# Kernel optimization log

Measured on AMD Instinct MI355X. Metric: run time of the kernel, lower is better.

The kernel has to match this reference:

```python
import jax, jax.numpy as jnp
import numpy as np

D = 512
H = 8
G = 4          # GroupNorm groups
EPS = 1e-3     # GroupNorm eps


def group_norm(x):
    # x: (b, n, t, d); torch code normalizes per (batch, group) over (n*t, d/G)
    b, n, t, d = x.shape
    xr = x.reshape(b, n * t, G, d // G)
    mu = xr.mean(axis=(1, 3), keepdims=True)
    var = ((xr - mu) ** 2).mean(axis=(1, 3), keepdims=True)
    return ((xr - mu) * jax.lax.rsqrt(var + EPS)).reshape(b, n, t, d)


def setup_inputs() -> dict:
    key = jax.random.key(0)
    ks = jax.random.split(key, 9)
    s = 1.0 / np.sqrt(D)
    inp = {
        "ind": 0,
        "in_f": jax.random.normal(ks[0], (4, 8, 512, D), dtype=jnp.float32),
        "in_f_kv": jax.random.normal(ks[1], (4, 8, 512, D), dtype=jnp.float32),
        "Wq": jax.random.normal(ks[2], (D, D), dtype=jnp.float32) * s,
        "Wk": jax.random.normal(ks[3], (D, D), dtype=jnp.float32) * s,
        "Wv": jax.random.normal(ks[4], (D, D), dtype=jnp.float32) * s,
        "Wz": jax.random.normal(ks[5], (D, D), dtype=jnp.float32) * s,
        "bz": jnp.zeros((D,), dtype=jnp.float32),
        "W1": jax.random.normal(ks[6], (D, D), dtype=jnp.float32) * s,
        "b1": jnp.full((D,), 0.1, dtype=jnp.float32),
        "W2": jax.random.normal(ks[7], (D, D), dtype=jnp.float32) * s,
        "b2": jnp.full((D,), 0.1, dtype=jnp.float32),
    }
    return inp


def reference(ind, in_f, in_f_kv, Wq, Wk, Wv, Wz, bz, W1, b1, W2, b2):
    b, n, t, d = in_f.shape
    hd = d // H
    scale = 1.0 / np.sqrt(hd)

    _in_f = group_norm(in_f)          # LN_1
    _in_f_kv = group_norm(in_f_kv)    # LN_2

    # torch Linear: y = x @ W.T
    q = group_norm(_in_f @ Wq.T)      # LN_3
    k = group_norm(_in_f_kv @ Wk.T)   # LN_4
    v = _in_f_kv @ Wv.T

    q = q.reshape(b, n, t, H, hd)
    k = k.reshape(b, n, -1, H, hd)
    v = v.reshape(b, n, -1, H, hd)

    logits = jnp.einsum('bnqhd,bnkhd->bnhqk', q, k) * scale
    attn_weights = jax.nn.softmax(logits, axis=-1)
    attn_out = jnp.einsum('bnhqk,bnkhd->bnqhd', attn_weights, v).reshape(b, n, t, d)

    in_f_u1 = attn_out @ Wz.T + bz
    in_f_u2 = jax.nn.leaky_relu(_in_f @ W1.T + b1, negative_slope=0.01) @ W2.T + b2

    out_f = in_f + in_f_u1 + in_f_u2
    return (out_f, attn_weights)
```

## Files before the change

kernel.cpp:

```cpp
#include <hip/hip_runtime.h>
#include <math.h>

#define TDIM 512
#define DDIM 512
#define NTROWS 4096
#define MROWS 16384
#define EPSGN 1e-3f

typedef __attribute__((ext_vector_type(8))) short bf16x8;
typedef __attribute__((ext_vector_type(4))) float f32x4;
typedef __attribute__((ext_vector_type(8))) unsigned short us8;
typedef __attribute__((ext_vector_type(4))) unsigned short us4;

__device__ __forceinline__ unsigned short f2b(float f) {
  unsigned int u = __float_as_uint(f);
  return (unsigned short)((u + 0x7fffu + ((u >> 16) & 1u)) >> 16);
}
__device__ __forceinline__ float b2f(unsigned short h) {
  return __uint_as_float(((unsigned int)h) << 16);
}

#define GLOAD16(g, l)                                                                   \
  __builtin_amdgcn_global_load_lds((const __attribute__((address_space(1))) void*)(g),  \
                                   (__attribute__((address_space(3))) void*)(l), 16, 0, 0)

__global__ __launch_bounds__(256) void gn_stats_partial(const float* __restrict__ x,
                                                        float* __restrict__ part) {
  const int grp = blockIdx.x;
  const int chunk = blockIdx.y;
  const int b = grp >> 2, g = grp & 3;
  const float* base = x + (size_t)b * NTROWS * DDIM + g * 128;
  const int r0 = chunk * (NTROWS / 32);
  float s = 0.f, sq = 0.f;
  for (int i = threadIdx.x; i < 128 * 32; i += 256) {
    const int r = i >> 5, c4 = (i & 31) << 2;
    const float4 v = *(const float4*)(base + (size_t)(r0 + r) * DDIM + c4);
    s += v.x + v.y + v.z + v.w;
    sq += v.x * v.x + v.y * v.y + v.z * v.z + v.w * v.w;
  }
#pragma unroll
  for (int o = 32; o > 0; o >>= 1) { s += __shfl_down(s, o); sq += __shfl_down(sq, o); }
  __shared__ float red[8];
  const int wid = threadIdx.x >> 6;
  if ((threadIdx.x & 63) == 0) { red[wid * 2] = s; red[wid * 2 + 1] = sq; }
  __syncthreads();
  if (threadIdx.x == 0) {
    float S = 0.f, SQ = 0.f;
    for (int w = 0; w < 4; ++w) { S += red[w * 2]; SQ += red[w * 2 + 1]; }
    part[(grp * 32 + chunk) * 2] = S;
    part[(grp * 32 + chunk) * 2 + 1] = SQ;
  }
}

__global__ __launch_bounds__(256) void cvt_gn(const float* __restrict__ x,
                                              const float* __restrict__ part,
                                              unsigned short* __restrict__ o) {
  __shared__ float sstat[32];
  if (threadIdx.x < 16) {
    const float* p = part + threadIdx.x * 64;
    float S = 0.f, SQ = 0.f;
    for (int c = 0; c < 32; ++c) { S += p[c * 2]; SQ += p[c * 2 + 1]; }
    const float inv = 1.f / (float)(NTROWS * 128);
    const float mu = S * inv;
    const float var = SQ * inv - mu * mu;
    sstat[threadIdx.x * 2] = mu;
    sstat[threadIdx.x * 2 + 1] = rsqrtf(var + EPSGN);
  }
  __syncthreads();
  const int NC = MROWS * DDIM / 8;
  for (int c = blockIdx.x * 256 + threadIdx.x; c < NC; c += gridDim.x * 256) {
    const int e = c * 8;
    const int row = e >> 9;
    const int ch = e & 511;
    const int sidx = (((row >> 12) << 2) | (ch >> 7)) << 1;
    const float mu = sstat[sidx], rs = sstat[sidx + 1];
    const float4 f0 = *(const float4*)(x + (size_t)e);
    const float4 f1 = *(const float4*)(x + (size_t)e + 4);
    us8 v;
    v[0] = f2b((f0.x - mu) * rs); v[1] = f2b((f0.y - mu) * rs);
    v[2] = f2b((f0.z - mu) * rs); v[3] = f2b((f0.w - mu) * rs);
    v[4] = f2b((f1.x - mu) * rs); v[5] = f2b((f1.y - mu) * rs);
    v[6] = f2b((f1.z - mu) * rs); v[7] = f2b((f1.w - mu) * rs);
    *(us8*)(o + (size_t)e) = v;
  }
}

__global__ __launch_bounds__(256) void cvt_w(const float* w0, const float* w1, const float* w2,
                                             const float* w3, const float* w4, const float* w5,
                                             unsigned short* __restrict__ dst) {
  const float* s;
  switch (blockIdx.y) {
    case 0: s = w0; break; case 1: s = w1; break; case 2: s = w2; break;
    case 3: s = w3; break; case 4: s = w4; break; default: s = w5; break;
  }
  unsigned short* d = dst + (size_t)blockIdx.y * 262144;
  const int c = blockIdx.x * 256 + threadIdx.x;
  const float4 f0 = *(const float4*)(s + (size_t)c * 8);
  const float4 f1 = *(const float4*)(s + (size_t)c * 8 + 4);
  us8 o;
  o[0] = f2b(f0.x); o[1] = f2b(f0.y); o[2] = f2b(f0.z); o[3] = f2b(f0.w);
  o[4] = f2b(f1.x); o[5] = f2b(f1.y); o[6] = f2b(f1.z); o[7] = f2b(f1.w);
  *(us8*)(d + (size_t)c * 8) = o;
}

template <int EPI, int STATS>
__global__ __launch_bounds__(256) void gemm_bf16(const unsigned short* __restrict__ A,
                                                 const unsigned short* __restrict__ B,
                                                 unsigned short* __restrict__ Cb,
                                                 const float* __restrict__ bias,
                                                 float* __restrict__ part) {
  __shared__ __align__(16) unsigned short As[128 * 64];
  __shared__ __align__(16) unsigned short Bs[128 * 64];
  const int tid = threadIdx.x;
  const int wave = tid >> 6, lane = tid & 63;
  const int bm = blockIdx.x << 7, bn = blockIdx.y << 7;
  const int wr = (wave >> 1) << 6;
  const int wc = (wave & 1) << 6;
  const int lr = lane & 15, lg = lane >> 4;

  f32x4 acc[4][4] = {};

  const int srow = lane >> 3;
  const int sslot = (lane & 7) ^ srow;

  for (int k0 = 0; k0 < 512; k0 += 64) {
    __syncthreads();
#pragma unroll
    for (int i = 0; i < 4; ++i) {
      const int ci = wave * 4 + i;
      const int row = ci * 8 + srow;
      GLOAD16(A + (size_t)(bm + row) * 512 + k0 + sslot * 8, (char*)As + ci * 1024);
      GLOAD16(B + (size_t)(bn + row) * 512 + k0 + sslot * 8, (char*)Bs + ci * 1024);
    }
    __syncthreads();
#pragma unroll
    for (int kk = 0; kk < 64; kk += 32) {
      bf16x8 af[4], bfr[4];
#pragma unroll
      for (int i = 0; i < 4; ++i) {
        const int row = wr + i * 16 + lr;
        af[i] = *(const bf16x8*)&As[row * 64 + ((((kk >> 3) + lg) ^ (row & 7)) << 3)];
      }
#pragma unroll
      for (int j = 0; j < 4; ++j) {
        const int row = wc + j * 16 + lr;
        bfr[j] = *(const bf16x8*)&Bs[row * 64 + ((((kk >> 3) + lg) ^ (row & 7)) << 3)];
      }
#pragma unroll
      for (int i = 0; i < 4; ++i)
#pragma unroll
        for (int j = 0; j < 4; ++j)
          acc[i][j] = __builtin_amdgcn_mfma_f32_16x16x32_bf16(af[i], bfr[j], acc[i][j], 0, 0, 0);
    }
  }

#pragma unroll
  for (int i = 0; i < 4; ++i) {
    const int row0 = bm + wr + i * 16 + lg * 4;
#pragma unroll
    for (int j = 0; j < 4; ++j) {
      const int col = bn + wc + j * 16 + lr;
      if (EPI == 0) {
#pragma unroll
        for (int r = 0; r < 4; ++r)
          Cb[(size_t)(row0 + r) * 512 + col] = f2b(acc[i][j][r]);
      } else if (EPI == 1) {
        const float bb = bias[col];
#pragma unroll
        for (int r = 0; r < 4; ++r) {
          float v = acc[i][j][r] + bb;
          v = v > 0.f ? v : 0.01f * v;
          Cb[(size_t)(row0 + r) * 512 + col] = f2b(v);
        }
      } else {
        us4 pk;
#pragma unroll
        for (int r = 0; r < 4; ++r) pk[r] = f2b(acc[i][j][r]);
        *(us4*)&Cb[((size_t)(row0 >> 9) * 512 + col) * 512 + (row0 & 511)] = pk;
      }
    }
  }

  if (STATS) {
    float s = 0.f, sq = 0.f;
#pragma unroll
    for (int i = 0; i < 4; ++i)
#pragma unroll
      for (int j = 0; j < 4; ++j)
#pragma unroll
        for (int r = 0; r < 4; ++r) { const float v = acc[i][j][r]; s += v; sq += v * v; }
#pragma unroll
    for (int o = 32; o > 0; o >>= 1) { s += __shfl_xor(s, o); sq += __shfl_xor(sq, o); }
    __shared__ float red[8];
    if (lane == 0) { red[wave * 2] = s; red[wave * 2 + 1] = sq; }
    __syncthreads();
    if (tid == 0) {
      const float S = red[0] + red[2] + red[4] + red[6];
      const float SQ = red[1] + red[3] + red[5] + red[7];
      const int batch = blockIdx.x >> 5, slot = blockIdx.x & 31, g = blockIdx.y;
      const int idx = ((((batch << 2) | g) << 5) | slot) << 1;
      part[idx] = S;
      part[idx + 1] = SQ;
    }
  }
}

__global__ __launch_bounds__(256) void gemm_final(const unsigned short* __restrict__ A0,
                                                  const unsigned short* __restrict__ A1,
                                                  const unsigned short* __restrict__ B0,
                                                  const unsigned short* __restrict__ B1,
                                                  float* __restrict__ Cf,
                                                  const float* __restrict__ bias0,
                                                  const float* __restrict__ bias1,
                                                  const float* __restrict__ init) {
  __shared__ __align__(16) unsigned short As[128 * 64];
  __shared__ __align__(16) unsigned short Bs[128 * 64];
  const int tid = threadIdx.x;
  const int wave = tid >> 6, lane = tid & 63;
  const int bm = blockIdx.x << 7, bn = blockIdx.y << 7;
  const int wr = (wave >> 1) << 6;
  const int wc = (wave & 1) << 6;
  const int lr = lane & 15, lg = lane >> 4;

  f32x4 acc[4][4] = {};
  const int srow = lane >> 3;
  const int sslot = (lane & 7) ^ srow;

  for (int k0 = 0; k0 < 1024; k0 += 64) {
    const unsigned short* Ab = (k0 < 512) ? A0 : A1;
    const unsigned short* Bb = (k0 < 512) ? B0 : B1;
    const int kl = k0 & 511;
    __syncthreads();
#pragma unroll
    for (int i = 0; i < 4; ++i) {
      const int ci = wave * 4 + i;
      const int row = ci * 8 + srow;
      GLOAD16(Ab + (size_t)(bm + row) * 512 + kl + sslot * 8, (char*)As + ci * 1024);
      GLOAD16(Bb + (size_t)(bn + row) * 512 + kl + sslot * 8, (char*)Bs + ci * 1024);
    }
    __syncthreads();
#pragma unroll
    for (int kk = 0; kk < 64; kk += 32) {
      bf16x8 af[4], bfr[4];
#pragma unroll
      for (int i = 0; i < 4; ++i) {
        const int row = wr + i * 16 + lr;
        af[i] = *(const bf16x8*)&As[row * 64 + ((((kk >> 3) + lg) ^ (row & 7)) << 3)];
      }
#pragma unroll
      for (int j = 0; j < 4; ++j) {
        const int row = wc + j * 16 + lr;
        bfr[j] = *(const bf16x8*)&Bs[row * 64 + ((((kk >> 3) + lg) ^ (row & 7)) << 3)];
      }
#pragma unroll
      for (int i = 0; i < 4; ++i)
#pragma unroll
        for (int j = 0; j < 4; ++j)
          acc[i][j] = __builtin_amdgcn_mfma_f32_16x16x32_bf16(af[i], bfr[j], acc[i][j], 0, 0, 0);
    }
  }

#pragma unroll
  for (int i = 0; i < 4; ++i) {
    const int row0 = bm + wr + i * 16 + lg * 4;
#pragma unroll
    for (int j = 0; j < 4; ++j) {
      const int col = bn + wc + j * 16 + lr;
      const float bb = bias0[col] + bias1[col];
#pragma unroll
      for (int r = 0; r < 4; ++r) {
        const size_t o = (size_t)(row0 + r) * 512 + col;
        Cf[o] = acc[i][j][r] + bb + init[o];
      }
    }
  }
}

__global__ __launch_bounds__(256) void attn_fused(const unsigned short* __restrict__ q16,
                                                  const unsigned short* __restrict__ k16,
                                                  const unsigned short* __restrict__ vT,
                                                  const float* __restrict__ part_q,
                                                  const float* __restrict__ part_k,
                                                  float* __restrict__ aw,
                                                  unsigned short* __restrict__ ao16) {
  __shared__ __align__(16) unsigned short Qs[64 * 64];
  __shared__ __align__(16) unsigned short Ks[256 * 64];
  __shared__ __align__(16) unsigned short Ps[64 * 256];
  __shared__ float WM[4][64];
  __shared__ float WS[4][64];
  __shared__ float sstat[4];

  const int bid = blockIdx.x;
  const int q0 = blockIdx.y << 6;
  const int h = bid & 7;
  const int b = bid >> 6;
  const int tid = threadIdx.x;
  const int w = tid >> 6, lane = tid & 63;
  const int lr = lane & 15, lg = lane >> 4;

  if (tid < 2) {
    const float* p = (tid == 0 ? part_q : part_k) + ((((b << 2) | (h >> 1)) << 5) << 1);
    float S = 0.f, SQ = 0.f;
    for (int c = 0; c < 32; ++c) { S += p[c * 2]; SQ += p[c * 2 + 1]; }
    const float inv = 1.f / (float)(NTROWS * 128);
    const float mu = S * inv;
    const float var = SQ * inv - mu * mu;
    sstat[tid * 2] = mu;
    sstat[tid * 2 + 1] = rsqrtf(var + EPSGN);
  }
  __syncthreads();
  const float qmu = sstat[0], qrs = sstat[1], kmu = sstat[2], krs = sstat[3];

  const size_t hb = (size_t)(bid >> 3) * (512 * 512);
  const unsigned short* Qg = q16 + hb + h * 64;
  const unsigned short* Kg = k16 + hb + h * 64;
  const unsigned short* Vg = vT + hb + (size_t)h * 64 * 512;

  {
    const int row = tid >> 2, cb = (tid & 3) << 4;
    const us8 v0 = *(const us8*)(Qg + (size_t)(q0 + row) * 512 + cb);
    const us8 v1 = *(const us8*)(Qg + (size_t)(q0 + row) * 512 + cb + 8);
    us8 o0, o1;
#pragma unroll
    for (int j = 0; j < 8; ++j) {
      o0[j] = f2b((b2f(v0[j]) - qmu) * qrs);
      o1[j] = f2b((b2f(v1[j]) - qmu) * qrs);
    }
    const int s0 = (cb >> 3) ^ (row & 7);
    const int s1 = ((cb >> 3) + 1) ^ (row & 7);
    *(us8*)&Qs[row * 64 + (s0 << 3)] = o0;
    *(us8*)&Qs[row * 64 + (s1 << 3)] = o1;
  }

  f32x4 sc[4][8] = {};

#pragma unroll
  for (int half = 0; half < 2; ++half) {
    __syncthreads();
#pragma unroll
    for (int it = 0; it < 8; ++it) {
      const int row = it * 32 + (tid >> 3), slot = tid & 7;
      const us8 v = *(const us8*)(Kg + (size_t)(half * 256 + row) * 512 + (slot << 3));
      us8 o;
#pragma unroll
      for (int j = 0; j < 8; ++j) o[j] = f2b((b2f(v[j]) - kmu) * krs);
      *(us8*)&Ks[row * 64 + ((slot ^ (row & 7)) << 3)] = o;
    }
    __syncthreads();
#pragma unroll
    for (int kk = 0; kk < 64; kk += 32) {
      bf16x8 aq[4];
#pragma unroll
      for (int qf = 0; qf < 4; ++qf) {
        const int row = qf * 16 + lr;
        aq[qf] = *(const bf16x8*)&Qs[row * 64 + ((((kk >> 3) + lg) ^ (row & 7)) << 3)];
      }
#pragma unroll
      for (int kf = 0; kf < 4; ++kf) {
        const int row = w * 64 + kf * 16 + lr;
        const bf16x8 bk = *(const bf16x8*)&Ks[row * 64 + ((((kk >> 3) + lg) ^ (row & 7)) << 3)];
#pragma unroll
        for (int qf = 0; qf < 4; ++qf)
          sc[qf][half * 4 + kf] =
              __builtin_amdgcn_mfma_f32_16x16x32_bf16(aq[qf], bk, sc[qf][half * 4 + kf], 0, 0, 0);
      }
    }
  }

  float Mv[4][4];
#pragma unroll
  for (int qf = 0; qf < 4; ++qf)
#pragma unroll
    for (int r = 0; r < 4; ++r) {
      float m = sc[qf][0][r];
#pragma unroll
      for (int kf = 1; kf < 8; ++kf) m = fmaxf(m, sc[qf][kf][r]);
#pragma unroll
      for (int o = 1; o < 16; o <<= 1) m = fmaxf(m, __shfl_xor(m, o));
      Mv[qf][r] = m;
    }
  if (lr == 0) {
#pragma unroll
    for (int qf = 0; qf < 4; ++qf)
#pragma unroll
      for (int r = 0; r < 4; ++r) WM[w][qf * 16 + lg * 4 + r] = Mv[qf][r];
  }
  __syncthreads();
#pragma unroll
  for (int qf = 0; qf < 4; ++qf)
#pragma unroll
    for (int r = 0; r < 4; ++r) {
      const int q = qf * 16 + lg * 4 + r;
      Mv[qf][r] = fmaxf(fmaxf(WM[0][q], WM[1][q]), fmaxf(WM[2][q], WM[3][q]));
    }
  float sl[4][4] = {};
#pragma unroll
  for (int qf = 0; qf < 4; ++qf)
#pragma unroll
    for (int kf = 0; kf < 8; ++kf) {
      f32x4 v = sc[qf][kf];
#pragma unroll
      for (int r = 0; r < 4; ++r) {
        const float e = __expf((v[r] - Mv[qf][r]) * 0.125f);
        v[r] = e;
        sl[qf][r] += e;
      }
      sc[qf][kf] = v;
    }
#pragma unroll
  for (int qf = 0; qf < 4; ++qf)
#pragma unroll
    for (int r = 0; r < 4; ++r) {
      float s = sl[qf][r];
#pragma unroll
      for (int o = 1; o < 16; o <<= 1) s += __shfl_xor(s, o);
      sl[qf][r] = s;
    }
  if (lr == 0) {
#pragma unroll
    for (int qf = 0; qf < 4; ++qf)
#pragma unroll
      for (int r = 0; r < 4; ++r) WS[w][qf * 16 + lg * 4 + r] = sl[qf][r];
  }
  __syncthreads();
#pragma unroll
  for (int qf = 0; qf < 4; ++qf)
#pragma unroll
    for (int r = 0; r < 4; ++r) {
      const int q = qf * 16 + lg * 4 + r;
      const float inv = 1.f / (WS[0][q] + WS[1][q] + WS[2][q] + WS[3][q]);
#pragma unroll
      for (int kf = 0; kf < 8; ++kf) sc[qf][kf][r] *= inv;
    }

  float* AWp = aw + ((size_t)bid * 512 + q0) * 512;
#pragma unroll
  for (int qf = 0; qf < 4; ++qf)
#pragma unroll
    for (int kfi = 0; kfi < 8; ++kfi) {
      const int k = ((kfi >> 2) << 8) + w * 64 + ((kfi & 3) << 4) + lr;
#pragma unroll
      for (int r = 0; r < 4; ++r)
        AWp[(size_t)(qf * 16 + lg * 4 + r) * 512 + k] = sc[qf][kfi][r];
    }

  f32x4 accO[4] = {};
#pragma unroll
  for (int half = 0; half < 2; ++half) {
    __syncthreads();
#pragma unroll
    for (int it = 0; it < 8; ++it) {
      const int ci = w * 8 + it;
      const int row = ci * 2 + (lane >> 5);
      const int s = lane & 31;
      GLOAD16(Vg + (size_t)row * 512 + half * 256 + ((s ^ (row & 7)) << 3),
              (char*)Ks + ci * 1024);
    }
#pragma unroll
    for (int qf = 0; qf < 4; ++qf)
#pragma unroll
      for (int r = 0; r < 4; ++r) {
        const int q = qf * 16 + lg * 4 + r;
#pragma unroll
        for (int kf = 0; kf < 4; ++kf) {
          const int k = w * 64 + (kf << 4) + lr;
          Ps[q * 256 + (((k >> 3) ^ (q & 7)) << 3) + (k & 7)] = f2b(sc[qf][half * 4 + kf][r]);
        }
      }
    __syncthreads();
#pragma unroll
    for (int ks = 0; ks < 256; ks += 32) {
      const int sl0 = ks >> 3;
      const int q = w * 16 + lr;
      const bf16x8 af = *(const bf16x8*)&Ps[q * 256 + (((sl0 + lg) ^ (q & 7)) << 3)];
#pragma unroll
      for (int df = 0; df < 4; ++df) {
        const int row = df * 16 + lr;
        const bf16x8 vb = *(const bf16x8*)&Ks[row * 256 + (((sl0 + lg) ^ (row & 7)) << 3)];
        accO[df] = __builtin_amdgcn_mfma_f32_16x16x32_bf16(af, vb, accO[df], 0, 0, 0);
      }
    }
  }

  const int growb = (bid >> 3) * 512 + q0 + w * 16 + lg * 4;
#pragma unroll
  for (int df = 0; df < 4; ++df)
#pragma unroll
    for (int r = 0; r < 4; ++r)
      ao16[(size_t)(growb + r) * 512 + h * 64 + df * 16 + lr] = f2b(accO[df][r]);
}

extern "C" void kernel_launch(void* const* d_in, const int* in_sizes, int n_in,
                              void* d_out, int out_size, void* d_ws, size_t ws_size,
                              hipStream_t stream) {
  const float* in_f = (const float*)d_in[1];
  const float* in_fkv = (const float*)d_in[2];
  const float* Wq = (const float*)d_in[3];
  const float* Wk = (const float*)d_in[4];
  const float* Wv = (const float*)d_in[5];
  const float* Wz = (const float*)d_in[6];
  const float* bz = (const float*)d_in[7];
  const float* W1 = (const float*)d_in[8];
  const float* b1 = (const float*)d_in[9];
  const float* W2 = (const float*)d_in[10];
  const float* b2 = (const float*)d_in[11];

  float* out_f = (float*)d_out;
  float* attw = out_f + (size_t)MROWS * DDIM;

  const size_t TSB = (size_t)MROWS * DDIM;
  unsigned short* us = (unsigned short*)d_ws;
  unsigned short* a16 = us;
  unsigned short* akv16 = us + TSB;
  unsigned short* q16 = us + 2 * TSB;
  unsigned short* k16 = us + 3 * TSB;
  unsigned short* h16 = us + 4 * TSB;
  unsigned short* ao16 = us + 5 * TSB;
  unsigned short* vT = us + 6 * TSB;
  unsigned short* w16 = us + 7 * TSB;
  float* fbase = (float*)(us + 7 * TSB + 6 * 262144);
  float* part0 = fbase;
  float* part1 = fbase + 1024;
  float* part_q = fbase + 2048;
  float* part_k = fbase + 3072;

  dim3 sg(16, 32);
  gn_stats_partial<<<sg, 256, 0, stream>>>(in_f, part0);
  gn_stats_partial<<<sg, 256, 0, stream>>>(in_fkv, part1);
  cvt_gn<<<2048, 256, 0, stream>>>(in_f, part0, a16);
  cvt_gn<<<2048, 256, 0, stream>>>(in_fkv, part1, akv16);
  cvt_w<<<dim3(128, 6), 256, 0, stream>>>(Wq, Wk, Wv, Wz, W1, W2, w16);

  dim3 gg(128, 4);
  gemm_bf16<0, 1><<<gg, 256, 0, stream>>>(a16, w16 + 0 * 262144, q16, nullptr, part_q);
  gemm_bf16<0, 1><<<gg, 256, 0, stream>>>(akv16, w16 + 1 * 262144, k16, nullptr, part_k);
  gemm_bf16<2, 0><<<gg, 256, 0, stream>>>(akv16, w16 + 2 * 262144, vT, nullptr, nullptr);
  gemm_bf16<1, 0><<<gg, 256, 0, stream>>>(a16, w16 + 4 * 262144, h16, b1, nullptr);

  attn_fused<<<dim3(256, 8), 256, 0, stream>>>(q16, k16, vT, part_q, part_k, attw, ao16);

  gemm_final<<<gg, 256, 0, stream>>>(ao16, h16, w16 + 3 * 262144, w16 + 5 * 262144, out_f, bz,
                                     b2, in_f);
}
```

Baseline: 287.1 us.

## Batch paired launches and move Q/K GroupNorm out of attention into separate pass

Merges the two stats and two convert launches into single launches that pick their inputs by grid index, and fuses the four projection GEMMs into two paired launches that share an A operand across a doubled grid. Q/K group normalization moves out of the attention kernel into a standalone in-place norm_qk pass. The attention kernel can then load Q and K tiles straight into LDS with async global-to-LDS loads. This cuts launch overhead and per-block normalization work inside attention, at the cost of an extra read-write pass over q16 and k16.

```diff
diff --git a/kernel.cpp b/kernel.cpp
--- a/kernel.cpp
+++ b/kernel.cpp
@@ -24,8 +24,12 @@
   __builtin_amdgcn_global_load_lds((const __attribute__((address_space(1))) void*)(g),  \
                                    (__attribute__((address_space(3))) void*)(l), 16, 0, 0)
 
-__global__ __launch_bounds__(256) void gn_stats_partial(const float* __restrict__ x,
-                                                        float* __restrict__ part) {
+__global__ __launch_bounds__(256) void gn_stats_partial(const float* __restrict__ x0,
+                                                        const float* __restrict__ x1,
+                                                        float* __restrict__ p0,
+                                                        float* __restrict__ p1) {
+  const float* x = blockIdx.z ? x1 : x0;
+  float* part = blockIdx.z ? p1 : p0;
   const int grp = blockIdx.x;
   const int chunk = blockIdx.y;
   const int b = grp >> 2, g = grp & 3;
@@ -52,9 +56,15 @@
   }
 }
 
-__global__ __launch_bounds__(256) void cvt_gn(const float* __restrict__ x,
-                                              const float* __restrict__ part,
-                                              unsigned short* __restrict__ o) {
+__global__ __launch_bounds__(256) void cvt_gn(const float* __restrict__ x0,
+                                              const float* __restrict__ x1,
+                                              const float* __restrict__ p0,
+                                              const float* __restrict__ p1,
+                                              unsigned short* __restrict__ o0,
+                                              unsigned short* __restrict__ o1) {
+  const float* x = blockIdx.y ? x1 : x0;
+  const float* part = blockIdx.y ? p1 : p0;
+  unsigned short* o = blockIdx.y ? o1 : o0;
   __shared__ float sstat[32];
   if (threadIdx.x < 16) {
     const float* p = part + threadIdx.x * 64;
@@ -103,23 +113,27 @@
   *(us8*)(d + (size_t)c * 8) = o;
 }
 
-template <int EPI, int STATS>
-__global__ __launch_bounds__(256) void gemm_bf16(const unsigned short* __restrict__ A,
-                                                 const unsigned short* __restrict__ B,
-                                                 unsigned short* __restrict__ Cb,
+template <int PAIR>
+__global__ __launch_bounds__(256) void gemm_pair(const unsigned short* __restrict__ A,
+                                                 const unsigned short* __restrict__ B0,
+                                                 const unsigned short* __restrict__ B1,
+                                                 unsigned short* __restrict__ C0,
+                                                 unsigned short* __restrict__ C1,
                                                  const float* __restrict__ bias,
                                                  float* __restrict__ part) {
   __shared__ __align__(16) unsigned short As[128 * 64];
   __shared__ __align__(16) unsigned short Bs[128 * 64];
   const int tid = threadIdx.x;
   const int wave = tid >> 6, lane = tid & 63;
-  const int bm = blockIdx.x << 7, bn = blockIdx.y << 7;
+  const int bm = blockIdx.x << 7;
+  const bool first = blockIdx.y < 4;
+  const unsigned short* B = first ? B0 : B1;
+  const int bnl = (blockIdx.y & 3) << 7;
   const int wr = (wave >> 1) << 6;
   const int wc = (wave & 1) << 6;
   const int lr = lane & 15, lg = lane >> 4;
 
   f32x4 acc[4][4] = {};
-
   const int srow = lane >> 3;
   const int sslot = (lane & 7) ^ srow;
 
@@ -130,7 +144,7 @@
       const int ci = wave * 4 + i;
       const int row = ci * 8 + srow;
       GLOAD16(A + (size_t)(bm + row) * 512 + k0 + sslot * 8, (char*)As + ci * 1024);
-      GLOAD16(B + (size_t)(bn + row) * 512 + k0 + sslot * 8, (char*)Bs + ci * 1024);
+      GLOAD16(B + (size_t)(bnl + row) * 512 + k0 + sslot * 8, (char*)Bs + ci * 1024);
     }
     __syncthreads();
 #pragma unroll
@@ -154,34 +168,18 @@
     }
   }
 
-#pragma unroll
-  for (int i = 0; i < 4; ++i) {
-    const int row0 = bm + wr + i * 16 + lg * 4;
-#pragma unroll
-    for (int j = 0; j < 4; ++j) {
-      const int col = bn + wc + j * 16 + lr;
-      if (EPI == 0) {
+  if (first) {
+#pragma unroll
+    for (int i = 0; i < 4; ++i) {
+      const int row0 = bm + wr + i * 16 + lg * 4;
+#pragma unroll
+      for (int j = 0; j < 4; ++j) {
+        const int col = bnl + wc + j * 16 + lr;
 #pragma unroll
         for (int r = 0; r < 4; ++r)
-          Cb[(size_t)(row0 + r) * 512 + col] = f2b(acc[i][j][r]);
-      } else if (EPI == 1) {
-        const float bb = bias[col];
-#pragma unroll
-        for (int r = 0; r < 4; ++r) {
-          float v = acc[i][j][r] + bb;
-          v = v > 0.f ? v : 0.01f * v;
-          Cb[(size_t)(row0 + r) * 512 + col] = f2b(v);
-        }
-      } else {
-        us4 pk;
-#pragma unroll
-        for (int r = 0; r < 4; ++r) pk[r] = f2b(acc[i][j][r]);
-        *(us4*)&Cb[((size_t)(row0 >> 9) * 512 + col) * 512 + (row0 & 511)] = pk;
-      }
-    }
-  }
-
-  if (STATS) {
+          C0[(size_t)(row0 + r) * 512 + col] = f2b(acc[i][j][r]);
+      }
+    }
     float s = 0.f, sq = 0.f;
 #pragma unroll
     for (int i = 0; i < 4; ++i)
@@ -202,7 +200,65 @@
       part[idx] = S;
       part[idx + 1] = SQ;
     }
-  }
+  } else if (PAIR == 0) {
+#pragma unroll
+    for (int i = 0; i < 4; ++i) {
+      const int row0 = bm + wr + i * 16 + lg * 4;
+#pragma unroll
+      for (int j = 0; j < 4; ++j) {
+        const int col = bnl + wc + j * 16 + lr;
+        const float bb = bias[col];
+#pragma unroll
+        for (int r = 0; r < 4; ++r) {
+          float v = acc[i][j][r] + bb;
+          v = v > 0.f ? v : 0.01f * v;
+          C1[(size_t)(row0 + r) * 512 + col] = f2b(v);
+        }
+      }
+    }
+  } else {
+#pragma unroll
+    for (int i = 0; i < 4; ++i) {
+      const int row0 = bm + wr + i * 16 + lg * 4;
+#pragma unroll
+      for (int j = 0; j < 4; ++j) {
+        const int col = bnl + wc + j * 16 + lr;
+        us4 pk;
+#pragma unroll
+        for (int r = 0; r < 4; ++r) pk[r] = f2b(acc[i][j][r]);
+        *(us4*)&C1[((size_t)(row0 >> 9) * 512 + col) * 512 + (row0 & 511)] = pk;
+      }
+    }
+  }
+}
+
+__global__ __launch_bounds__(256) void norm_qk(unsigned short* __restrict__ q,
+                                               unsigned short* __restrict__ k,
+                                               const float* __restrict__ pq,
+                                               const float* __restrict__ pk) {
+  unsigned short* x = blockIdx.y ? k : q;
+  const float* part = blockIdx.y ? pk : pq;
+  const int e0 = blockIdx.x << 11;
+  const int batch = blockIdx.x >> 10;
+  __shared__ float st[8];
+  if (threadIdx.x < 4) {
+    const float* p = part + (((batch << 2) | threadIdx.x) << 6);
+    float S = 0.f, SQ = 0.f;
+    for (int c = 0; c < 32; ++c) { S += p[c * 2]; SQ += p[c * 2 + 1]; }
+    const float inv = 1.f / (float)(NTROWS * 128);
+    const float mu = S * inv;
+    const float var = SQ * inv - mu * mu;
+    st[threadIdx.x * 2] = mu;
+    st[threadIdx.x * 2 + 1] = rsqrtf(var + EPSGN);
+  }
+  __syncthreads();
+  const int e = e0 + threadIdx.x * 8;
+  const int g = (e & 511) >> 7;
+  const float mu = st[g * 2], rs = st[g * 2 + 1];
+  us8 v = *(const us8*)(x + (size_t)e);
+#pragma unroll
+  for (int j = 0; j < 8; ++j) v[j] = f2b((b2f(v[j]) - mu) * rs);
+  *(us8*)(x + (size_t)e) = v;
 }
 
 __global__ __launch_bounds__(256) void gemm_final(const unsigned short* __restrict__ A0,
@@ -279,8 +335,6 @@
 __global__ __launch_bounds__(256) void attn_fused(const unsigned short* __restrict__ q16,
                                                   const unsigned short* __restrict__ k16,
                                                   const unsigned short* __restrict__ vT,
-                                                  const float* __restrict__ part_q,
-                                                  const float* __restrict__ part_k,
                                                   float* __restrict__ aw,
                                                   unsigned short* __restrict__ ao16) {
   __shared__ __align__(16) unsigned short Qs[64 * 64];
@@ -288,48 +342,26 @@
   __shared__ __align__(16) unsigned short Ps[64 * 256];
   __shared__ float WM[4][64];
   __shared__ float WS[4][64];
-  __shared__ float sstat[4];
 
   const int bid = blockIdx.x;
   const int q0 = blockIdx.y << 6;
   const int h = bid & 7;
-  const int b = bid >> 6;
   const int tid = threadIdx.x;
   const int w = tid >> 6, lane = tid & 63;
   const int lr = lane & 15, lg = lane >> 4;
-
-  if (tid < 2) {
-    const float* p = (tid == 0 ? part_q : part_k) + ((((b << 2) | (h >> 1)) << 5) << 1);
-    float S = 0.f, SQ = 0.f;
-    for (int c = 0; c < 32; ++c) { S += p[c * 2]; SQ += p[c * 2 + 1]; }
-    const float inv = 1.f / (float)(NTROWS * 128);
-    const float mu = S * inv;
-    const float var = SQ * inv - mu * mu;
-    sstat[tid * 2] = mu;
-    sstat[tid * 2 + 1] = rsqrtf(var + EPSGN);
-  }
-  __syncthreads();
-  const float qmu = sstat[0], qrs = sstat[1], kmu = sstat[2], krs = sstat[3];
+  const int srow = lane >> 3;
+  const int sslot = (lane & 7) ^ srow;
 
   const size_t hb = (size_t)(bid >> 3) * (512 * 512);
   const unsigned short* Qg = q16 + hb + h * 64;
   const unsigned short* Kg = k16 + hb + h * 64;
   const unsigned short* Vg = vT + hb + (size_t)h * 64 * 512;
 
-  {
-    const int row = tid >> 2, cb = (tid & 3) << 4;
-    const us8 v0 = *(const us8*)(Qg + (size_t)(q0 + row) * 512 + cb);
-    const us8 v1 = *(const us8*)(Qg + (size_t)(q0 + row) * 512 + cb + 8);
-    us8 o0, o1;
-#pragma unroll
-    for (int j = 0; j < 8; ++j) {
-      o0[j] = f2b((b2f(v0[j]) - qmu) * qrs);
-      o1[j] = f2b((b2f(v1[j]) - qmu) * qrs);
-    }
-    const int s0 = (cb >> 3) ^ (row & 7);
-    const int s1 = ((cb >> 3) + 1) ^ (row & 7);
-    *(us8*)&Qs[row * 64 + (s0 << 3)] = o0;
-    *(us8*)&Qs[row * 64 + (s1 << 3)] = o1;
+#pragma unroll
+  for (int it = 0; it < 2; ++it) {
+    const int ci = w * 2 + it;
+    const int row = ci * 8 + srow;
+    GLOAD16(Qg + (size_t)(q0 + row) * 512 + sslot * 8, (char*)Qs + ci * 1024);
   }
 
   f32x4 sc[4][8] = {};
@@ -339,12 +371,9 @@
     __syncthreads();
 #pragma unroll
     for (int it = 0; it < 8; ++it) {
-      const int row = it * 32 + (tid >> 3), slot = tid & 7;
-      const us8 v = *(const us8*)(Kg + (size_t)(half * 256 + row) * 512 + (slot << 3));
-      us8 o;
-#pragma unroll
-      for (int j = 0; j < 8; ++j) o[j] = f2b((b2f(v[j]) - kmu) * krs);
-      *(us8*)&Ks[row * 64 + ((slot ^ (row & 7)) << 3)] = o;
+      const int ci = w * 8 + it;
+      const int row = ci * 8 + srow;
+      GLOAD16(Kg + (size_t)(half * 256 + row) * 512 + sslot * 8, (char*)Ks + ci * 1024);
     }
     __syncthreads();
 #pragma unroll
@@ -524,21 +553,19 @@
   float* part_q = fbase + 2048;
   float* part_k = fbase + 3072;
 
-  dim3 sg(16, 32);
-  gn_stats_partial<<<sg, 256, 0, stream>>>(in_f, part0);
-  gn_stats_partial<<<sg, 256, 0, stream>>>(in_fkv, part1);
-  cvt_gn<<<2048, 256, 0, stream>>>(in_f, part0, a16);
-  cvt_gn<<<2048, 256, 0, stream>>>(in_fkv, part1, akv16);
+  gn_stats_partial<<<dim3(16, 32, 2), 256, 0, stream>>>(in_f, in_fkv, part0, part1);
+  cvt_gn<<<dim3(2048, 2), 256, 0, stream>>>(in_f, in_fkv, part0, part1, a16, akv16);
   cvt_w<<<dim3(128, 6), 256, 0, stream>>>(Wq, Wk, Wv, Wz, W1, W2, w16);
 
-  dim3 gg(128, 4);
-  gemm_bf16<0, 1><<<gg, 256, 0, stream>>>(a16, w16 + 0 * 262144, q16, nullptr, part_q);
-  gemm_bf16<0, 1><<<gg, 256, 0, stream>>>(akv16, w16 + 1 * 262144, k16, nullptr, part_k);
-  gemm_bf16<2, 0><<<gg, 256, 0, stream>>>(akv16, w16 + 2 * 262144, vT, nullptr, nullptr);
-  gemm_bf16<1, 0><<<gg, 256, 0, stream>>>(a16, w16 + 4 * 262144, h16, b1, nullptr);
-
-  attn_fused<<<dim3(256, 8), 256, 0, stream>>>(q16, k16, vT, part_q, part_k, attw, ao16);
-
-  gemm_final<<<gg, 256, 0, stream>>>(ao16, h16, w16 + 3 * 262144, w16 + 5 * 262144, out_f, bz,
-                                     b2, in_f);
-}
+  gemm_pair<0><<<dim3(128, 8), 256, 0, stream>>>(a16, w16 + 0 * 262144, w16 + 4 * 262144, q16,
+                                                 h16, b1, part_q);
+  gemm_pair<1><<<dim3(128, 8), 256, 0, stream>>>(akv16, w16 + 1 * 262144, w16 + 2 * 262144, k16,
+                                                 vT, nullptr, part_k);
+
+  norm_qk<<<dim3(4096, 2), 256, 0, stream>>>(q16, k16, part_q, part_k);
+
+  attn_fused<<<dim3(256, 8), 256, 0, stream>>>(q16, k16, vT, attw, ao16);
+
+  gemm_final<<<dim3(128, 4), 256, 0, stream>>>(ao16, h16, w16 + 3 * 262144, w16 + 5 * 262144,
+                                               out_f, bz, b2, in_f);
+}
```

New measurement: 309.3 us. 1.08x slower.
